# Optimization experiments

Hardware: AMD Instinct MI355X
Metric: run time of the kernel (lower is better)

## Reference

```python
import jax, jax.numpy as jnp
import numpy as np
import math

N_USER = 50000
N_ITEM = 50000
E = 400000
IN_DIM = 128
OUT_DIM = 128
H = 4
DK = OUT_DIM // H
LN_EPS = 1e-5


def setup_inputs() -> dict:
    key = jax.random.key(0)
    ks = jax.random.split(key, 24)
    w = lambda k, shp: (jax.random.normal(k, shp, dtype=jnp.float32) * 0.05)
    inp = {
        'x_user': jax.random.normal(ks[0], (N_USER, IN_DIM), dtype=jnp.float32),
        'x_item': jax.random.normal(ks[1], (N_ITEM, IN_DIM), dtype=jnp.float32),
        'ei_ui': jax.random.randint(ks[2], (2, E), 0, N_USER),   # user -> item
        'ei_iu': jax.random.randint(ks[3], (2, E), 0, N_ITEM),   # item -> user
        'Wk_user': w(ks[4], (IN_DIM, OUT_DIM)),
        'Wq_user': w(ks[5], (IN_DIM, OUT_DIM)),
        'Wv_user': w(ks[6], (IN_DIM, OUT_DIM)),
        'Wk_item': w(ks[7], (IN_DIM, OUT_DIM)),
        'Wq_item': w(ks[8], (IN_DIM, OUT_DIM)),
        'Wv_item': w(ks[9], (IN_DIM, OUT_DIM)),
        'Wa_ui': w(ks[10], (OUT_DIM, H)),
        'Wa_iu': w(ks[11], (OUT_DIM, H)),
        'Wm_user': w(ks[12], (OUT_DIM, OUT_DIM)),
        'bm_user': jnp.zeros((OUT_DIM,), jnp.float32),
        'Wm_item': w(ks[13], (OUT_DIM, OUT_DIM)),
        'bm_item': jnp.zeros((OUT_DIM,), jnp.float32),
        'Wg_user': w(ks[14], (OUT_DIM, OUT_DIM)),
        'bg_user': jnp.zeros((OUT_DIM,), jnp.float32),
        'Wg_item': w(ks[15], (OUT_DIM, OUT_DIM)),
        'bg_item': jnp.zeros((OUT_DIM,), jnp.float32),
        'lng_user': jnp.ones((OUT_DIM,), jnp.float32),
        'lnb_user': jnp.zeros((OUT_DIM,), jnp.float32),
        'lng_item': jnp.ones((OUT_DIM,), jnp.float32),
        'lnb_item': jnp.zeros((OUT_DIM,), jnp.float32),
    }
    return inp


def _edge_type_messages(k_src, v_src, q_dst, ei, Wa, num_dst):
    # Per-edge-type gather K/Q/V, attention over heads, scatter-add aggregation.
    src, dst = ei[0], ei[1]
    ek = k_src[src]                                     # [E, out]
    eq = q_dst[dst]                                     # [E, out]
    scores = (ek.reshape(-1, H, DK) * eq.reshape(-1, H, DK)).sum(-1) / math.sqrt(DK)
    scores = scores + ek @ Wa                           # [E, H]
    attn = jax.nn.softmax(scores, axis=-1)              # softmax over HEADS (as in source)
    ev = v_src[src].reshape(-1, H, DK)
    attended = (attn[..., None] * ev).reshape(-1, OUT_DIM)
    msg = jax.ops.segment_sum(attended, dst, num_segments=num_dst)
    wsum = jax.ops.segment_sum(attn.sum(-1), dst, num_segments=num_dst)
    return msg, wsum


def _layer_norm(x, g, b):
    mu = x.mean(-1, keepdims=True)
    var = ((x - mu) ** 2).mean(-1, keepdims=True)
    return (x - mu) * jax.lax.rsqrt(var + LN_EPS) * g + b


def reference(x_user, x_item, ei_ui, ei_iu,
              Wk_user, Wq_user, Wv_user, Wk_item, Wq_item, Wv_item,
              Wa_ui, Wa_iu,
              Wm_user, bm_user, Wm_item, bm_item,
              Wg_user, bg_user, Wg_item, bg_item,
              lng_user, lnb_user, lng_item, lnb_item):
    # K/Q/V projections per node type
    k_user, q_user, v_user = x_user @ Wk_user, x_user @ Wq_user, x_user @ Wv_user
    k_item, q_item, v_item = x_item @ Wk_item, x_item @ Wq_item, x_item @ Wv_item

    # dst = item: edges user->item
    msg_i, ws_i = _edge_type_messages(k_user, v_user, q_item, ei_ui, Wa_ui, N_ITEM)
    agg_i = msg_i / jnp.clip(ws_i, 1e-8)[:, None]
    h_i = (agg_i @ Wm_item + bm_item) @ Wg_item + bg_item
    out_item = _layer_norm(h_i + x_item, lng_item, lnb_item)

    # dst = user: edges item->user
    msg_u, ws_u = _edge_type_messages(k_item, v_item, q_user, ei_iu, Wa_iu, N_USER)
    agg_u = msg_u / jnp.clip(ws_u, 1e-8)[:, None]
    h_u = (agg_u @ Wm_user + bm_user) @ Wg_user + bg_user
    out_user = _layer_norm(h_u + x_user, lng_user, lnb_user)

    return jnp.stack([out_user, out_item])  # [2, N, out]
```

## Files before the change

kernel.cpp:

```cpp
#include <hip/hip_runtime.h>
#include <hip/hip_bf16.h>

#define DIM 128

typedef short s16x8 __attribute__((ext_vector_type(8)));
typedef float f32x4 __attribute__((ext_vector_type(4)));

__device__ __forceinline__ ushort f2b(float f) {
    __hip_bfloat16 h = __float2bfloat16(f);
    return *reinterpret_cast<ushort*>(&h);
}
__device__ __forceinline__ uint pk2(float a, float b) {
    return (uint)f2b(a) | ((uint)f2b(b) << 16);
}
__device__ __forceinline__ float bl(uint u) { return __uint_as_float(u << 16); }
__device__ __forceinline__ float bh(uint u) { return __uint_as_float(u & 0xffff0000u); }

__device__ __forceinline__ int swz(int row, int kelem) {
    int b = row * 256 + kelem * 2;
    return b ^ ((row & 7) << 4);
}
__device__ __forceinline__ s16x8 read_frag(const char* lds, int row, int k0) {
    return *(const s16x8*)(lds + swz(row, k0));
}

struct WPtrs { const float* w[10]; };

__global__ __launch_bounds__(256) void prep_hist(
    WPtrs p, ushort* __restrict__ out,
    const int* __restrict__ dst_i, const int* __restrict__ dst_u,
    int* __restrict__ cnt, int ni, int E)
{
    const int id = blockIdx.x * 256 + threadIdx.x;
    if (id < 20480) {
        const int m = id >> 11;
        const int c = id & 2047;
        const int lane = c & 63;
        const int kb = (c >> 6) & 3;
        const int ct = (c >> 8) & 1;
        const int w = (c >> 9) & 3;
        const int n = w * 32 + ct * 16 + (lane & 15);
        const int k0 = kb * 32 + 8 * (lane >> 4);
        const float* W = p.w[m];
        float v[8];
#pragma unroll
        for (int j = 0; j < 8; ++j) v[j] = W[(size_t)(k0 + j) * 128 + n];
        uint4 u;
        u.x = pk2(v[0], v[1]); u.y = pk2(v[2], v[3]);
        u.z = pk2(v[4], v[5]); u.w = pk2(v[6], v[7]);
        *(uint4*)&out[((size_t)m * 2048 + c) * 8] = u;
    } else {
        const int gid = id - 20480;
        if (gid < E) atomicAdd(&cnt[dst_i[gid]], 1);
        else if (gid < 2 * E) atomicAdd(&cnt[ni + dst_u[gid - E]], 1);
    }
}

__device__ __forceinline__ void load_bfrag_pk(const ushort* __restrict__ Wf,
                                              s16x8 B[2][4], int w, int l) {
#pragma unroll
    for (int ct = 0; ct < 2; ++ct)
#pragma unroll
        for (int kb = 0; kb < 4; ++kb)
            B[ct][kb] = *(const s16x8*)&Wf[(size_t)(((w * 2 + ct) * 4 + kb) * 64 + l) * 8];
}

__device__ __forceinline__ void stage_f32(const float* __restrict__ src, int r0, int N, char* lds) {
    const int t = threadIdx.x;
    const int r = t >> 2;
    const int k0 = (t & 3) * 32;
    const int row = r0 + r;
#pragma unroll
    for (int c = 0; c < 4; ++c) {
        uint4 u = make_uint4(0, 0, 0, 0);
        if (row < N) {
            const float4 f0 = *(const float4*)&src[(size_t)row * 128 + k0 + c * 8];
            const float4 f1 = *(const float4*)&src[(size_t)row * 128 + k0 + c * 8 + 4];
            u.x = pk2(f0.x, f0.y); u.y = pk2(f0.z, f0.w);
            u.z = pk2(f1.x, f1.y); u.w = pk2(f1.z, f1.w);
        }
        *(uint4*)(lds + swz(r, k0 + c * 8)) = u;
    }
}

__device__ __forceinline__ void stage_b16(const ushort* __restrict__ src, int r0, int N, char* lds) {
    const int t = threadIdx.x;
    const int r = t >> 2;
    const int k0 = (t & 3) * 32;
    const int row = r0 + r;
#pragma unroll
    for (int c = 0; c < 4; ++c) {
        uint4 u = make_uint4(0, 0, 0, 0);
        if (row < N) u = *(const uint4*)&src[(size_t)row * 128 + k0 + c * 8];
        *(uint4*)(lds + swz(r, k0 + c * 8)) = u;
    }
}

template<typename IT>
__global__ __launch_bounds__(256, 4) void proj_scatter(
    const int* __restrict__ ei_ui, const int* __restrict__ ei_iu,
    int* __restrict__ fill, IT* __restrict__ bucket, int histB, int E,
    const float* __restrict__ xu, const ushort* __restrict__ wfrag,
    const float* __restrict__ Waui,
    ushort* __restrict__ Ku, ushort* __restrict__ Qu, ushort* __restrict__ Vu,
    float* __restrict__ kwa_u, int n_user, int ntu,
    const float* __restrict__ xi,
    const float* __restrict__ Waiu,
    ushort* __restrict__ Ki, ushort* __restrict__ Qi, ushort* __restrict__ Vi,
    float* __restrict__ kwa_i, int n_item)
{
    __shared__ char at[16384];
    __shared__ float kwp[4][64][4];
    const int b = blockIdx.x;

    if (b < histB) {
        const int e = b * 256 + threadIdx.x;
        if (e < E) {
            const int pos = atomicAdd(&fill[ei_ui[E + e]], 1);
            bucket[pos] = (IT)ei_ui[e];
        } else if (e < 2 * E) {
            const int pos = atomicAdd(&fill[n_item + ei_iu[e]], 1);
            bucket[pos] = (IT)ei_iu[e - E];
        }
        return;
    }

    const int bb = b - histB;
    const int m = bb % 3;
    const int tile = bb / 3;
    const bool user = tile < ntu;
    const float* x = user ? xu : xi;
    const int N = user ? n_user : n_item;
    const int tl = user ? tile : tile - ntu;
    const ushort* WF = wfrag + (size_t)(user ? m : m + 3) * 16384;
    ushort* O = user ? (m == 0 ? Ku : (m == 1 ? Qu : Vu))
                     : (m == 0 ? Ki : (m == 1 ? Qi : Vi));
    const float* Wa = user ? Waui : Waiu;
    float* kwa = user ? kwa_u : kwa_i;

    const int t = threadIdx.x, w = t >> 6, l = t & 63;
    const int lr = l & 15, lg = l >> 4;
    const int r0 = tl << 6;

    stage_f32(x, r0, N, at);
    __syncthreads();

    const int col0 = w * 32 + lr, col1 = col0 + 16;
    s16x8 B[2][4];
    load_bfrag_pk(WF, B, w, l);

    if (m == 0) {
        const float4 waA = *(const float4*)&Wa[col0 * 4];
        const float4 waB = *(const float4*)&Wa[col1 * 4];
#pragma unroll
        for (int rt = 0; rt < 4; ++rt) {
            s16x8 af[4];
#pragma unroll
            for (int kb = 0; kb < 4; ++kb)
                af[kb] = read_frag(at, rt * 16 + lr, kb * 32 + 8 * lg);
            const int rbase = r0 + rt * 16 + 4 * lg;
            f32x4 a0 = {0.f, 0.f, 0.f, 0.f}, a1 = {0.f, 0.f, 0.f, 0.f};
#pragma unroll
            for (int kb = 0; kb < 4; ++kb) {
                a0 = __builtin_amdgcn_mfma_f32_16x16x32_bf16(af[kb], B[0][kb], a0, 0, 0, 0);
                a1 = __builtin_amdgcn_mfma_f32_16x16x32_bf16(af[kb], B[1][kb], a1, 0, 0, 0);
            }
#pragma unroll
            for (int j = 0; j < 4; ++j) {
                if (rbase + j < N) {
                    O[(size_t)(rbase + j) * 128 + col0] = f2b(a0[j]);
                    O[(size_t)(rbase + j) * 128 + col1] = f2b(a1[j]);
                }
            }
#pragma unroll
            for (int j = 0; j < 4; ++j) {
                float p0 = a0[j] * waA.x + a1[j] * waB.x;
                float p1 = a0[j] * waA.y + a1[j] * waB.y;
                float p2 = a0[j] * waA.z + a1[j] * waB.z;
                float p3 = a0[j] * waA.w + a1[j] * waB.w;
#pragma unroll
                for (int off = 8; off; off >>= 1) {
                    p0 += __shfl_xor(p0, off);
                    p1 += __shfl_xor(p1, off);
                    p2 += __shfl_xor(p2, off);
                    p3 += __shfl_xor(p3, off);
                }
                if (lr == 0) {
                    kwp[w][rt * 16 + 4 * lg + j][0] = p0;
                    kwp[w][rt * 16 + 4 * lg + j][1] = p1;
                    kwp[w][rt * 16 + 4 * lg + j][2] = p2;
                    kwp[w][rt * 16 + 4 * lg + j][3] = p3;
                }
            }
        }
        __syncthreads();
        if (t < 64 && r0 + t < N) {
            const float s0 = kwp[0][t][0] + kwp[1][t][0] + kwp[2][t][0] + kwp[3][t][0];
            const float s1 = kwp[0][t][1] + kwp[1][t][1] + kwp[2][t][1] + kwp[3][t][1];
            const float s2 = kwp[0][t][2] + kwp[1][t][2] + kwp[2][t][2] + kwp[3][t][2];
            const float s3 = kwp[0][t][3] + kwp[1][t][3] + kwp[2][t][3] + kwp[3][t][3];
            *(float4*)&kwa[(size_t)(r0 + t) * 4] = make_float4(s0, s1, s2, s3);
        }
    } else {
#pragma unroll
        for (int rt = 0; rt < 4; ++rt) {
            s16x8 af[4];
#pragma unroll
            for (int kb = 0; kb < 4; ++kb)
                af[kb] = read_frag(at, rt * 16 + lr, kb * 32 + 8 * lg);
            const int rbase = r0 + rt * 16 + 4 * lg;
            f32x4 a0 = {0.f, 0.f, 0.f, 0.f}, a1 = {0.f, 0.f, 0.f, 0.f};
#pragma unroll
            for (int kb = 0; kb < 4; ++kb) {
                a0 = __builtin_amdgcn_mfma_f32_16x16x32_bf16(af[kb], B[0][kb], a0, 0, 0, 0);
                a1 = __builtin_amdgcn_mfma_f32_16x16x32_bf16(af[kb], B[1][kb], a1, 0, 0, 0);
            }
#pragma unroll
            for (int j = 0; j < 4; ++j) {
                if (rbase + j < N) {
                    O[(size_t)(rbase + j) * 128 + col0] = f2b(a0[j]);
                    O[(size_t)(rbase + j) * 128 + col1] = f2b(a1[j]);
                }
            }
        }
    }
}

__global__ __launch_bounds__(256) void alloc_kernel(
    const int* __restrict__ cnt, int* __restrict__ base,
    int* __restrict__ fill, int* __restrict__ cursor, int n)
{
    const int d = blockIdx.x * blockDim.x + threadIdx.x;
    const int lane = threadIdx.x & 63;
    int c = (d < n) ? cnt[d] : 0;
    int sc = c;
#pragma unroll
    for (int off = 1; off < 64; off <<= 1) {
        int t = __shfl_up(sc, off);
        if (lane >= off) sc += t;
    }
    const int total = __shfl(sc, 63);
    int wb = 0;
    if (lane == 63) wb = atomicAdd(cursor, total);
    wb = __shfl(wb, 63);
    if (d < n) {
        const int b = wb + sc - c;
        base[d] = b;
        fill[d] = b;
    }
}

__device__ __forceinline__ void unpack8(uint4 u, float* q) {
    q[0] = bl(u.x); q[1] = bh(u.x); q[2] = bl(u.y); q[3] = bh(u.y);
    q[4] = bl(u.z); q[5] = bh(u.z); q[6] = bl(u.w); q[7] = bh(u.w);
}
__device__ __forceinline__ float dot8(uint4 u, const float* q) {
    return bl(u.x) * q[0] + bh(u.x) * q[1] + bl(u.y) * q[2] + bh(u.y) * q[3]
         + bl(u.z) * q[4] + bh(u.z) * q[5] + bl(u.w) * q[6] + bh(u.w) * q[7];
}
__device__ __forceinline__ void acc8(uint4 u, float a, float* acc) {
    acc[0] += a * bl(u.x); acc[1] += a * bh(u.x);
    acc[2] += a * bl(u.y); acc[3] += a * bh(u.y);
    acc[4] += a * bl(u.z); acc[5] += a * bh(u.z);
    acc[6] += a * bl(u.w); acc[7] += a * bh(u.w);
}

template<typename IT>
__global__ __launch_bounds__(256, 4) void agg8_kernel(
    const int* __restrict__ base, const int* __restrict__ cnt, const IT* __restrict__ bsrc,
    const ushort* __restrict__ Ku, const ushort* __restrict__ Qi, const ushort* __restrict__ Vu,
    const float* __restrict__ kwa_u, ushort* __restrict__ msgA,
    const ushort* __restrict__ Ki, const ushort* __restrict__ Qu, const ushort* __restrict__ Vi,
    const float* __restrict__ kwa_i, ushort* __restrict__ msgB,
    int n_item, int ntot)
{
    const int gid = (int)((blockIdx.x * blockDim.x + threadIdx.x) >> 3);
    if (gid >= ntot) return;
    const int li = threadIdx.x & 7;
    const bool item_side = gid < n_item;
    const int d = item_side ? gid : gid - n_item;
    const ushort* K  = item_side ? Ku : Ki;
    const ushort* Q  = item_side ? Qi : Qu;
    const ushort* V  = item_side ? Vu : Vi;
    const float* kwa = item_side ? kwa_u : kwa_i;
    ushort* msg      = item_side ? msgA : msgB;

    const float inv = 0.17677669529663687f;
    const int doff = li * 16;
    const int h = li >> 1;

    float q[16];
    {
        const uint4* qp = (const uint4*)&Q[(size_t)d * 128 + doff];
        unpack8(qp[0], &q[0]);
        unpack8(qp[1], &q[8]);
    }
    float acc[16];
#pragma unroll
    for (int m = 0; m < 16; ++m) acc[m] = 0.f;

    const int b = base[gid], c = cnt[gid];
    uint4 kc0, kc1, vc0, vc1;
    float kwc;
    int s = 0;
    if (c > 0) {
        s = (int)bsrc[b];
        const uint4* kp = (const uint4*)&K[(size_t)s * 128 + doff];
        const uint4* vp = (const uint4*)&V[(size_t)s * 128 + doff];
        kc0 = kp[0]; kc1 = kp[1];
        vc0 = vp[0]; vc1 = vp[1];
        kwc = kwa[(size_t)s * 4 + h];
    }

    for (int i = 0; i < c; ++i) {
        const int sn = (i + 1 < c) ? (int)bsrc[b + i + 1] : s;
        const uint4* kp = (const uint4*)&K[(size_t)sn * 128 + doff];
        const uint4* vp = (const uint4*)&V[(size_t)sn * 128 + doff];
        const uint4 kn0 = kp[0], kn1 = kp[1];
        const uint4 vn0 = vp[0], vn1 = vp[1];
        const float kwn = kwa[(size_t)sn * 4 + h];

        float p = dot8(kc0, &q[0]) + dot8(kc1, &q[8]);
        p += __shfl_xor(p, 1);
        const float e = __expf(p * inv + kwc);
        float es = e + __shfl_xor(e, 2);
        es += __shfl_xor(es, 4);
        const float att = __fdividef(e, es);
        acc8(vc0, att, &acc[0]);
        acc8(vc1, att, &acc[8]);

        kc0 = kn0; kc1 = kn1; vc0 = vn0; vc1 = vn1; kwc = kwn;
    }

    uint4* mp = (uint4*)&msg[(size_t)d * 128 + doff];
    uint4 o0, o1;
    o0.x = pk2(acc[0], acc[1]);  o0.y = pk2(acc[2], acc[3]);
    o0.z = pk2(acc[4], acc[5]);  o0.w = pk2(acc[6], acc[7]);
    o1.x = pk2(acc[8], acc[9]);  o1.y = pk2(acc[10], acc[11]);
    o1.z = pk2(acc[12], acc[13]); o1.w = pk2(acc[14], acc[15]);
    mp[0] = o0;
    mp[1] = o1;
}

__device__ void post_body(
    const ushort* __restrict__ A, const int* __restrict__ deg,
    const ushort* __restrict__ WmF, const float* __restrict__ bm,
    const ushort* __restrict__ WgF, const float* __restrict__ bg,
    const float* __restrict__ resid, const float* __restrict__ gamma,
    const float* __restrict__ beta, float* __restrict__ out, int N, int tile, char* mem)
{
    const int t = threadIdx.x, w = t >> 6, l = t & 63;
    const int lr = l & 15, lg = l >> 4;
    char* at = mem;
    char* tt = mem + 16384;
    float2 (*part)[64] = (float2 (*)[64])(mem + 32768);
    float2* lnp = (float2*)(mem + 32768 + 2048);

    const int col0 = w * 32 + lr, col1 = col0 + 16;
    const int r0 = tile << 6;
    stage_b16(A, r0, N, at);
    __syncthreads();

    {
        s16x8 B[2][4];
        load_bfrag_pk(WmF, B, w, l);
        const float bm0 = bm[col0], bm1 = bm[col1];
#pragma unroll
        for (int rt = 0; rt < 4; ++rt) {
            s16x8 af[4];
#pragma unroll
            for (int kb = 0; kb < 4; ++kb)
                af[kb] = read_frag(at, rt * 16 + lr, kb * 32 + 8 * lg);
            const int rbase = r0 + rt * 16 + 4 * lg;
            float rs[4];
#pragma unroll
            for (int j = 0; j < 4; ++j)
                rs[j] = (rbase + j < N) ? 1.0f / fmaxf((float)deg[rbase + j], 1e-8f) : 0.f;
            f32x4 a0 = {0.f, 0.f, 0.f, 0.f}, a1 = {0.f, 0.f, 0.f, 0.f};
#pragma unroll
            for (int kb = 0; kb < 4; ++kb) {
                a0 = __builtin_amdgcn_mfma_f32_16x16x32_bf16(af[kb], B[0][kb], a0, 0, 0, 0);
                a1 = __builtin_amdgcn_mfma_f32_16x16x32_bf16(af[kb], B[1][kb], a1, 0, 0, 0);
            }
#pragma unroll
            for (int j = 0; j < 4; ++j) {
                *(ushort*)(tt + swz(rt * 16 + 4 * lg + j, col0)) = f2b(a0[j] * rs[j] + bm0);
                *(ushort*)(tt + swz(rt * 16 + 4 * lg + j, col1)) = f2b(a1[j] * rs[j] + bm1);
            }
        }
    }
    __syncthreads();

    float v[4][2][4];
    {
        s16x8 B[2][4];
        load_bfrag_pk(WgF, B, w, l);
        const float bg0 = bg[col0], bg1 = bg[col1];
#pragma unroll
        for (int rt = 0; rt < 4; ++rt) {
            s16x8 af[4];
#pragma unroll
            for (int kb = 0; kb < 4; ++kb)
                af[kb] = read_frag(tt, rt * 16 + lr, kb * 32 + 8 * lg);
            const int rbase = r0 + rt * 16 + 4 * lg;
            f32x4 a0 = {0.f, 0.f, 0.f, 0.f}, a1 = {0.f, 0.f, 0.f, 0.f};
#pragma unroll
            for (int kb = 0; kb < 4; ++kb) {
                a0 = __builtin_amdgcn_mfma_f32_16x16x32_bf16(af[kb], B[0][kb], a0, 0, 0, 0);
                a1 = __builtin_amdgcn_mfma_f32_16x16x32_bf16(af[kb], B[1][kb], a1, 0, 0, 0);
            }
#pragma unroll
            for (int j = 0; j < 4; ++j) {
                const bool ok = (rbase + j < N);
                const float rv0 = ok ? resid[(size_t)(rbase + j) * 128 + col0] : 0.f;
                const float rv1 = ok ? resid[(size_t)(rbase + j) * 128 + col1] : 0.f;
                v[rt][0][j] = a0[j] + bg0 + rv0;
                v[rt][1][j] = a1[j] + bg1 + rv1;
            }
        }
    }
#pragma unroll
    for (int rt = 0; rt < 4; ++rt)
#pragma unroll
        for (int j = 0; j < 4; ++j) {
            float s = v[rt][0][j] + v[rt][1][j];
            float q = v[rt][0][j] * v[rt][0][j] + v[rt][1][j] * v[rt][1][j];
            s += __shfl_xor(s, 8); q += __shfl_xor(q, 8);
            s += __shfl_xor(s, 4); q += __shfl_xor(q, 4);
            s += __shfl_xor(s, 2); q += __shfl_xor(q, 2);
            s += __shfl_xor(s, 1); q += __shfl_xor(q, 1);
            if (lr == 0) part[w][rt * 16 + 4 * lg + j] = make_float2(s, q);
        }
    __syncthreads();
    if (t < 64) {
        const float S = part[0][t].x + part[1][t].x + part[2][t].x + part[3][t].x;
        const float Qq = part[0][t].y + part[1][t].y + part[2][t].y + part[3][t].y;
        const float mu = S * (1.f / 128.f);
        const float var = Qq * (1.f / 128.f) - mu * mu;
        lnp[t] = make_float2(mu, rsqrtf(var + 1e-5f));
    }
    __syncthreads();
    const float g0 = gamma[col0], g1 = gamma[col1];
    const float be0 = beta[col0], be1 = beta[col1];
#pragma unroll
    for (int rt = 0; rt < 4; ++rt) {
        const int rbase = r0 + rt * 16 + 4 * lg;
#pragma unroll
        for (int j = 0; j < 4; ++j) {
            const float2 mp = lnp[rt * 16 + 4 * lg + j];
            if (rbase + j < N) {
                out[(size_t)(rbase + j) * 128 + col0] = (v[rt][0][j] - mp.x) * mp.y * g0 + be0;
                out[(size_t)(rbase + j) * 128 + col1] = (v[rt][1][j] - mp.x) * mp.y * g1 + be1;
            }
        }
    }
}

__global__ __launch_bounds__(256, 4) void post2_kernel(
    const ushort* __restrict__ msgA, const int* __restrict__ cnt_i,
    const ushort* __restrict__ wfrag,
    const float* __restrict__ bmi, const float* __restrict__ bgi,
    const float* __restrict__ xi, const float* __restrict__ lngi, const float* __restrict__ lnbi,
    float* __restrict__ out_item, int n_item, int nti,
    const ushort* __restrict__ msgB, const int* __restrict__ cnt_u,
    const float* __restrict__ bmu, const float* __restrict__ bgu,
    const float* __restrict__ xu, const float* __restrict__ lngu, const float* __restrict__ lnbu,
    float* __restrict__ out_user, int n_user)
{
    __shared__ char mem[32768 + 2048 + 512];
    const int b = blockIdx.x;
    if (b < nti)
        post_body(msgA, cnt_i, wfrag + 6 * 16384, bmi, wfrag + 7 * 16384, bgi,
                  xi, lngi, lnbi, out_item, n_item, b, mem);
    else
        post_body(msgB, cnt_u, wfrag + 8 * 16384, bmu, wfrag + 9 * 16384, bgu,
                  xu, lngu, lnbu, out_user, n_user, b - nti, mem);
}

extern "C" void kernel_launch(void* const* d_in, const int* in_sizes, int n_in,
                              void* d_out, int out_size, void* d_ws, size_t ws_size,
                              hipStream_t stream)
{
    const float* x_user  = (const float*)d_in[0];
    const float* x_item  = (const float*)d_in[1];
    const int*   ei_ui   = (const int*)d_in[2];
    const int*   ei_iu   = (const int*)d_in[3];
    const float* Wk_user = (const float*)d_in[4];
    const float* Wq_user = (const float*)d_in[5];
    const float* Wv_user = (const float*)d_in[6];
    const float* Wk_item = (const float*)d_in[7];
    const float* Wq_item = (const float*)d_in[8];
    const float* Wv_item = (const float*)d_in[9];
    const float* Wa_ui   = (const float*)d_in[10];
    const float* Wa_iu   = (const float*)d_in[11];
    const float* Wm_user = (const float*)d_in[12];
    const float* bm_user = (const float*)d_in[13];
    const float* Wm_item = (const float*)d_in[14];
    const float* bm_item = (const float*)d_in[15];
    const float* Wg_user = (const float*)d_in[16];
    const float* bg_user = (const float*)d_in[17];
    const float* Wg_item = (const float*)d_in[18];
    const float* bg_item = (const float*)d_in[19];
    const float* lng_user = (const float*)d_in[20];
    const float* lnb_user = (const float*)d_in[21];
    const float* lng_item = (const float*)d_in[22];
    const float* lnb_item = (const float*)d_in[23];

    const int n_user = in_sizes[0] / DIM;
    const int n_item = in_sizes[1] / DIM;
    const int E = in_sizes[2] / 2;
    const int nmax = (n_user > n_item) ? n_user : n_item;
    const int ntot = n_user + n_item;
    const size_t nf = (size_t)nmax * DIM;

    ushort* Ku   = (ushort*)d_ws;
    ushort* Qu   = Ku + nf;
    ushort* Vu   = Qu + nf;
    ushort* Ki   = Vu + nf;
    ushort* Qi   = Ki + nf;
    ushort* Vi   = Qi + nf;
    ushort* msgA = Vi + nf;
    ushort* msgB = msgA + nf;
    float* kwa_u = (float*)(msgB + nf);
    float* kwa_i = kwa_u + (size_t)nmax * 4;
    int* cnt     = (int*)(kwa_i + (size_t)nmax * 4);
    int* cursor  = cnt + ntot;
    int* basep   = cursor + 4;
    int* fill    = basep + ntot;
    ushort* bucket16 = (ushort*)(fill + ntot);
    ushort* wfrag    = bucket16 + 2 * (size_t)E;

    float* out_user = (float*)d_out;
    float* out_item = out_user + (size_t)n_user * DIM;

    const dim3 blk(256);
    const int ntu = (n_user + 63) / 64, nti = (n_item + 63) / 64;
    const int histB = (2 * E + 255) / 256;

    hipMemsetAsync(cnt, 0, ((size_t)ntot + 4) * sizeof(int), stream);

    WPtrs wp;
    wp.w[0] = Wk_user; wp.w[1] = Wq_user; wp.w[2] = Wv_user;
    wp.w[3] = Wk_item; wp.w[4] = Wq_item; wp.w[5] = Wv_item;
    wp.w[6] = Wm_item; wp.w[7] = Wg_item;
    wp.w[8] = Wm_user; wp.w[9] = Wg_user;
    prep_hist<<<80 + histB, blk, 0, stream>>>(wp, wfrag, ei_ui + E, ei_iu + E, cnt, n_item, E);

    alloc_kernel<<<(ntot + 255) / 256, blk, 0, stream>>>(cnt, basep, fill, cursor, ntot);

    const int projB = histB + 3 * (ntu + nti);
    const int aggB = (ntot * 8 + 255) / 256;
    if (nmax <= 65535) {
        proj_scatter<ushort><<<projB, blk, 0, stream>>>(
            ei_ui, ei_iu, fill, bucket16, histB, E,
            x_user, wfrag, Wa_ui, Ku, Qu, Vu, kwa_u, n_user, ntu,
            x_item, Wa_iu, Ki, Qi, Vi, kwa_i, n_item);
        agg8_kernel<ushort><<<aggB, blk, 0, stream>>>(
            basep, cnt, (const ushort*)bucket16,
            Ku, Qi, Vu, kwa_u, msgA,
            Ki, Qu, Vi, kwa_i, msgB,
            n_item, ntot);
    } else {
        int* bucket32 = (int*)bucket16;
        proj_scatter<int><<<projB, blk, 0, stream>>>(
            ei_ui, ei_iu, fill, bucket32, histB, E,
            x_user, wfrag, Wa_ui, Ku, Qu, Vu, kwa_u, n_user, ntu,
            x_item, Wa_iu, Ki, Qi, Vi, kwa_i, n_item);
        agg8_kernel<int><<<aggB, blk, 0, stream>>>(
            basep, cnt, (const int*)bucket32,
            Ku, Qi, Vu, kwa_u, msgA,
            Ki, Qu, Vi, kwa_i, msgB,
            n_item, ntot);
    }

    post2_kernel<<<nti + ntu, blk, 0, stream>>>(
        msgA, cnt, wfrag, bm_item, bg_item, x_item, lng_item, lnb_item, out_item, n_item, nti,
        msgB, cnt + n_item, bm_user, bg_user, x_user, lng_user, lnb_user, out_user, n_user);
}
```

Baseline: 282.5 us.

## Split fused post-processing kernel into separate Wm and Wg+LayerNorm kernels

Splits the single post kernel, which chained two 128x128 GEMMs through LDS, into two launches. The first kernel applies the Wm projection with degree normalization and writes a bf16 intermediate to global memory, reusing the Ku/Ki buffers. The second reads it back and applies Wg, the residual and LayerNorm. This lowers per-block LDS use and may raise occupancy, at the cost of an extra global round trip, an extra launch, and scattered 2-byte global stores.

After: 267.3 us. -5.4%, faster.

```diff
diff --git a/kernel.cpp b/kernel.cpp
--- a/kernel.cpp
+++ b/kernel.cpp
@@ -342,81 +342,120 @@
     mp[1] = o1;
 }
 
-__device__ void post_body(
-    const ushort* __restrict__ A, const int* __restrict__ deg,
-    const ushort* __restrict__ WmF, const float* __restrict__ bm,
-    const ushort* __restrict__ WgF, const float* __restrict__ bg,
-    const float* __restrict__ resid, const float* __restrict__ gamma,
-    const float* __restrict__ beta, float* __restrict__ out, int N, int tile, char* mem)
+__global__ __launch_bounds__(256, 4) void postm_kernel(
+    const ushort* __restrict__ msgA, const int* __restrict__ cnt_i,
+    const ushort* __restrict__ wfrag, const float* __restrict__ bmi,
+    ushort* __restrict__ tmpA, int n_item, int nti,
+    const ushort* __restrict__ msgB, const int* __restrict__ cnt_u,
+    const float* __restrict__ bmu, ushort* __restrict__ tmpB, int n_user)
 {
+    __shared__ char at[16384];
+    const int b = blockIdx.x;
+    const bool item = b < nti;
+    const ushort* A = item ? msgA : msgB;
+    const int* deg = item ? cnt_i : cnt_u;
+    const ushort* WF = wfrag + (size_t)(item ? 6 : 8) * 16384;
+    const float* bm = item ? bmi : bmu;
+    ushort* T = item ? tmpA : tmpB;
+    const int N = item ? n_item : n_user;
+    const int tile = item ? b : b - nti;
+
     const int t = threadIdx.x, w = t >> 6, l = t & 63;
     const int lr = l & 15, lg = l >> 4;
-    char* at = mem;
-    char* tt = mem + 16384;
-    float2 (*part)[64] = (float2 (*)[64])(mem + 32768);
-    float2* lnp = (float2*)(mem + 32768 + 2048);
-
-    const int col0 = w * 32 + lr, col1 = col0 + 16;
     const int r0 = tile << 6;
+
     stage_b16(A, r0, N, at);
     __syncthreads();
 
-    {
-        s16x8 B[2][4];
-        load_bfrag_pk(WmF, B, w, l);
-        const float bm0 = bm[col0], bm1 = bm[col1];
-#pragma unroll
-        for (int rt = 0; rt < 4; ++rt) {
-            s16x8 af[4];
-#pragma unroll
-            for (int kb = 0; kb < 4; ++kb)
-                af[kb] = read_frag(at, rt * 16 + lr, kb * 32 + 8 * lg);
-            const int rbase = r0 + rt * 16 + 4 * lg;
-            float rs[4];
-#pragma unroll
-            for (int j = 0; j < 4; ++j)
-                rs[j] = (rbase + j < N) ? 1.0f / fmaxf((float)deg[rbase + j], 1e-8f) : 0.f;
-            f32x4 a0 = {0.f, 0.f, 0.f, 0.f}, a1 = {0.f, 0.f, 0.f, 0.f};
-#pragma unroll
-            for (int kb = 0; kb < 4; ++kb) {
-                a0 = __builtin_amdgcn_mfma_f32_16x16x32_bf16(af[kb], B[0][kb], a0, 0, 0, 0);
-                a1 = __builtin_amdgcn_mfma_f32_16x16x32_bf16(af[kb], B[1][kb], a1, 0, 0, 0);
+    const int col0 = w * 32 + lr, col1 = col0 + 16;
+    s16x8 B[2][4];
+    load_bfrag_pk(WF, B, w, l);
+    const float bm0 = bm[col0], bm1 = bm[col1];
+
+#pragma unroll
+    for (int rt = 0; rt < 4; ++rt) {
+        s16x8 af[4];
+#pragma unroll
+        for (int kb = 0; kb < 4; ++kb)
+            af[kb] = read_frag(at, rt * 16 + lr, kb * 32 + 8 * lg);
+        const int rbase = r0 + rt * 16 + 4 * lg;
+        float rs[4];
+#pragma unroll
+        for (int j = 0; j < 4; ++j)
+            rs[j] = (rbase + j < N) ? 1.0f / fmaxf((float)deg[rbase + j], 1e-8f) : 0.f;
+        f32x4 a0 = {0.f, 0.f, 0.f, 0.f}, a1 = {0.f, 0.f, 0.f, 0.f};
+#pragma unroll
+        for (int kb = 0; kb < 4; ++kb) {
+            a0 = __builtin_amdgcn_mfma_f32_16x16x32_bf16(af[kb], B[0][kb], a0, 0, 0, 0);
+            a1 = __builtin_amdgcn_mfma_f32_16x16x32_bf16(af[kb], B[1][kb], a1, 0, 0, 0);
+        }
+#pragma unroll
+        for (int j = 0; j < 4; ++j) {
+            if (rbase + j < N) {
+                T[(size_t)(rbase + j) * 128 + col0] = f2b(a0[j] * rs[j] + bm0);
+                T[(size_t)(rbase + j) * 128 + col1] = f2b(a1[j] * rs[j] + bm1);
             }
-#pragma unroll
-            for (int j = 0; j < 4; ++j) {
-                *(ushort*)(tt + swz(rt * 16 + 4 * lg + j, col0)) = f2b(a0[j] * rs[j] + bm0);
-                *(ushort*)(tt + swz(rt * 16 + 4 * lg + j, col1)) = f2b(a1[j] * rs[j] + bm1);
-            }
-        }
-    }
+        }
+    }
+}
+
+__global__ void postg_kernel(
+    const ushort* __restrict__ tmpA, const ushort* __restrict__ wfrag,
+    const float* __restrict__ bgi, const float* __restrict__ xi,
+    const float* __restrict__ lngi, const float* __restrict__ lnbi,
+    float* __restrict__ out_item, int n_item, int nti,
+    const ushort* __restrict__ tmpB, const float* __restrict__ bgu,
+    const float* __restrict__ xu, const float* __restrict__ lngu,
+    const float* __restrict__ lnbu, float* __restrict__ out_user, int n_user)
+{
+    __shared__ char at[16384];
+    __shared__ float2 part[4][64];
+    __shared__ float2 lnp[64];
+    const int b = blockIdx.x;
+    const bool item = b < nti;
+    const ushort* A = item ? tmpA : tmpB;
+    const ushort* WF = wfrag + (size_t)(item ? 7 : 9) * 16384;
+    const float* bg = item ? bgi : bgu;
+    const float* resid = item ? xi : xu;
+    const float* gamma = item ? lngi : lngu;
+    const float* beta = item ? lnbi : lnbu;
+    float* out = item ? out_item : out_user;
+    const int N = item ? n_item : n_user;
+    const int tile = item ? b : b - nti;
+
+    const int t = threadIdx.x, w = t >> 6, l = t & 63;
+    const int lr = l & 15, lg = l >> 4;
+    const int r0 = tile << 6;
+
+    stage_b16(A, r0, N, at);
     __syncthreads();
 
+    const int col0 = w * 32 + lr, col1 = col0 + 16;
+    s16x8 B[2][4];
+    load_bfrag_pk(WF, B, w, l);
+    const float bg0 = bg[col0], bg1 = bg[col1];
+
     float v[4][2][4];
-    {
-        s16x8 B[2][4];
-        load_bfrag_pk(WgF, B, w, l);
-        const float bg0 = bg[col0], bg1 = bg[col1];
-#pragma unroll
-        for (int rt = 0; rt < 4; ++rt) {
-            s16x8 af[4];
-#pragma unroll
-            for (int kb = 0; kb < 4; ++kb)
-                af[kb] = read_frag(tt, rt * 16 + lr, kb * 32 + 8 * lg);
-            const int rbase = r0 + rt * 16 + 4 * lg;
-            f32x4 a0 = {0.f, 0.f, 0.f, 0.f}, a1 = {0.f, 0.f, 0.f, 0.f};
-#pragma unroll
-            for (int kb = 0; kb < 4; ++kb) {
-                a0 = __builtin_amdgcn_mfma_f32_16x16x32_bf16(af[kb], B[0][kb], a0, 0, 0, 0);
-                a1 = __builtin_amdgcn_mfma_f32_16x16x32_bf16(af[kb], B[1][kb], a1, 0, 0, 0);
-            }
-#pragma unroll
-            for (int j = 0; j < 4; ++j) {
-                const bool ok = (rbase + j < N);
-                const float rv0 = ok ? resid[(size_t)(rbase + j) * 128 + col0] : 0.f;
-                const float rv1 = ok ? resid[(size_t)(rbase + j) * 128 + col1] : 0.f;
-                v[rt][0][j] = a0[j] + bg0 + rv0;
-                v[rt][1][j] = a1[j] + bg1 + rv1;
-            }
+#pragma unroll
+    for (int rt = 0; rt < 4; ++rt) {
+        s16x8 af[4];
+#pragma unroll
+        for (int kb = 0; kb < 4; ++kb)
+            af[kb] = read_frag(at, rt * 16 + lr, kb * 32 + 8 * lg);
+        const int rbase = r0 + rt * 16 + 4 * lg;
+        f32x4 a0 = {0.f, 0.f, 0.f, 0.f}, a1 = {0.f, 0.f, 0.f, 0.f};
+#pragma unroll
+        for (int kb = 0; kb < 4; ++kb) {
+            a0 = __builtin_amdgcn_mfma_f32_16x16x32_bf16(af[kb], B[0][kb], a0, 0, 0, 0);
+            a1 = __builtin_amdgcn_mfma_f32_16x16x32_bf16(af[kb], B[1][kb], a1, 0, 0, 0);
+        }
+#pragma unroll
+        for (int j = 0; j < 4; ++j) {
+            const bool ok = (rbase + j < N);
+            const float rv0 = ok ? resid[(size_t)(rbase + j) * 128 + col0] : 0.f;
+            const float rv1 = ok ? resid[(size_t)(rbase + j) * 128 + col1] : 0.f;
+            v[rt][0][j] = a0[j] + bg0 + rv0;
+            v[rt][1][j] = a1[j] + bg1 + rv1;
         }
     }
 #pragma unroll
@@ -454,27 +493,6 @@
             }
         }
     }
-}
-
-__global__ __launch_bounds__(256, 4) void post2_kernel(
-    const ushort* __restrict__ msgA, const int* __restrict__ cnt_i,
-    const ushort* __restrict__ wfrag,
-    const float* __restrict__ bmi, const float* __restrict__ bgi,
-    const float* __restrict__ xi, const float* __restrict__ lngi, const float* __restrict__ lnbi,
-    float* __restrict__ out_item, int n_item, int nti,
-    const ushort* __restrict__ msgB, const int* __restrict__ cnt_u,
-    const float* __restrict__ bmu, const float* __restrict__ bgu,
-    const float* __restrict__ xu, const float* __restrict__ lngu, const float* __restrict__ lnbu,
-    float* __restrict__ out_user, int n_user)
-{
-    __shared__ char mem[32768 + 2048 + 512];
-    const int b = blockIdx.x;
-    if (b < nti)
-        post_body(msgA, cnt_i, wfrag + 6 * 16384, bmi, wfrag + 7 * 16384, bgi,
-                  xi, lngi, lnbi, out_item, n_item, b, mem);
-    else
-        post_body(msgB, cnt_u, wfrag + 8 * 16384, bmu, wfrag + 9 * 16384, bgu,
-                  xu, lngu, lnbu, out_user, n_user, b - nti, mem);
 }
 
 extern "C" void kernel_launch(void* const* d_in, const int* in_sizes, int n_in,
@@ -529,6 +547,8 @@
     int* fill    = basep + ntot;
     ushort* bucket16 = (ushort*)(fill + ntot);
     ushort* wfrag    = bucket16 + 2 * (size_t)E;
+    ushort* tmpA = Ku;
+    ushort* tmpB = Ki;
 
     float* out_user = (float*)d_out;
     float* out_item = out_user + (size_t)n_user * DIM;
@@ -573,7 +593,11 @@
             n_item, ntot);
     }
 
-    post2_kernel<<<nti + ntu, blk, 0, stream>>>(
-        msgA, cnt, wfrag, bm_item, bg_item, x_item, lng_item, lnb_item, out_item, n_item, nti,
-        msgB, cnt + n_item, bm_user, bg_user, x_user, lng_user, lnb_user, out_user, n_user);
-}
+    postm_kernel<<<nti + ntu, blk, 0, stream>>>(
+        msgA, cnt, wfrag, bm_item, tmpA, n_item, nti,
+        msgB, cnt + n_item, bm_user, tmpB, n_user);
+
+    postg_kernel<<<nti + ntu, blk, 0, stream>>>(
+        tmpA, wfrag, bg_item, x_item, lng_item, lnb_item, out_item, n_item, nti,
+        tmpB, bg_user, x_user, lng_user, lnb_user, out_user, n_user);
+}
```
